# Performance work log

Hardware: AMD Instinct MI355X
Metric: run time of the kernel (lower is better)

## Reference

```python
import jax, jax.numpy as jnp
import numpy as np

NB_CODE = 1024
N, CODE_DIM, T = 32, 512, 2048


def setup_inputs() -> dict:
    key = jax.random.key(0)
    k1, k2 = jax.random.split(key)
    x = jax.random.normal(k1, (N, CODE_DIM, T), dtype=jnp.float32)
    codebook = jax.random.normal(k2, (NB_CODE, CODE_DIM), dtype=jnp.float32)
    return {"x": x, "codebook": codebook}


def reference(x, codebook):
    n, c, t = x.shape
    # preprocess: 'n c t -> (n t) c'
    xf = jnp.transpose(x, (0, 2, 1)).reshape(n * t, c)  # (NT, C)
    dist = (
        jnp.sum(xf * xf, axis=-1, keepdims=True)
        - 2.0 * jnp.matmul(xf, codebook.T)
        + jnp.sum(codebook * codebook, axis=-1)[None, :]
    )
    # gumbel_sample(-distance) with training=False -> plain argmax(-dist) = argmin(dist)
    code_idx = jnp.argmin(dist, axis=-1)  # (NT,) int32
    # dequantize: embedding gather
    x_d = codebook[code_idx]  # (NT, C)
    # compute_perplexity (eval path)
    counts = jax.ops.segment_sum(
        jnp.ones_like(code_idx, dtype=jnp.float32), code_idx, num_segments=NB_CODE
    )
    prob = counts / jnp.sum(counts)
    perplexity = jnp.exp(-jnp.sum(prob * jnp.log(prob + 1e-7)))
    # commit loss against detached quantized codes
    commit_loss = jnp.mean(jnp.square(xf - jax.lax.stop_gradient(x_d)))
    # straight-through estimator
    x_st = xf + jax.lax.stop_gradient(x_d - xf)
    x_out = jnp.transpose(x_st.reshape(n, t, c), (0, 2, 1))  # (N, C, T)
    return x_out, commit_loss, perplexity
```

## Files before the change

### kernel.cpp

```cpp
#include <hip/hip_runtime.h>
#include <stdint.h>

#define N_  32
#define C_  512
#define T_  2048
#define NB  1024
#define NT  (N_ * T_)
#define GB_S 129

typedef _Float16 h8 __attribute__((ext_vector_type(8)));
typedef _Float16 h4 __attribute__((ext_vector_type(4)));
typedef float    f4 __attribute__((ext_vector_type(4)));

#define WS_COMMIT   0
#define WS_SUMSQ    8
#define WS_COUNTS   64
#define WS_CNORM    4224
#define WS_RMIN     8320
#define WS_CBH      532608
#define WS_CBL      1581184
#define WS_XTH      2629760
#define WS_XTL      69738624
#define WS_NEED     136847488ull

__device__ __forceinline__ void gll16(const void* g, void* l) {
    __builtin_amdgcn_global_load_lds((const __attribute__((address_space(1))) void*)g,
                                     (__attribute__((address_space(3))) void*)l, 16, 0, 0);
}

__global__ void k_initA(unsigned* ws32, unsigned long long* rmin) {
    int g = blockIdx.x * 256 + threadIdx.x;
    if (g < 1040) ws32[g] = 0u;
    rmin[g] = 0xFFFFFFFFFFFFFFFFull;
}

__global__ void k_initS(unsigned* ws32) {
    int g = blockIdx.x * 256 + threadIdx.x;
    if (g < 1040) ws32[g] = 0u;
}

__global__ void k_codenorm(const float* __restrict__ cb, float* __restrict__ cnorm) {
    int j = blockIdx.x * 256 + threadIdx.x;
    const float* r = cb + (size_t)j * C_;
    float s = 0.f;
    for (int i = 0; i < C_; i += 4) {
        float4 v = *(const float4*)&r[i];
        s = fmaf(v.x, v.x, s); s = fmaf(v.y, v.y, s);
        s = fmaf(v.z, v.z, s); s = fmaf(v.w, v.w, s);
    }
    cnorm[j] = s;
}

__global__ void k_cvt_cb(const float* __restrict__ cb,
                         _Float16* __restrict__ cbh, _Float16* __restrict__ cbl) {
    int t = blockIdx.x * 256 + threadIdx.x;
    float4 v = *(const float4*)&cb[(size_t)t * 4];
    h4 hi, lo;
    hi.x = (_Float16)v.x; lo.x = (_Float16)(v.x - (float)hi.x);
    hi.y = (_Float16)v.y; lo.y = (_Float16)(v.y - (float)hi.y);
    hi.z = (_Float16)v.z; lo.z = (_Float16)(v.z - (float)hi.z);
    hi.w = (_Float16)v.w; lo.w = (_Float16)(v.w - (float)hi.w);
    *(h4*)&cbh[(size_t)t * 4] = hi;
    *(h4*)&cbl[(size_t)t * 4] = lo;
}

__global__ __launch_bounds__(256)
void k_xt(const float* __restrict__ x,
          _Float16* __restrict__ xth, _Float16* __restrict__ xtl,
          float* __restrict__ sumsq) {
    __shared__ float Ls[64 * 68];
    __shared__ float sred[4];
    const int bx = blockIdx.x;
    const int n = bx >> 8;
    const int cblk = (bx >> 5) & 7, tblk = bx & 31;
    const int c0 = cblk * 64, t0 = tblk * 64;
    const int tid = threadIdx.x;
    #pragma unroll
    for (int ld = 0; ld < 4; ++ld) {
        int idx = tid + ld * 256;
        int cc = idx >> 4, t4 = (idx & 15) << 2;
        float4 v = *(const float4*)&x[((size_t)n * C_ + c0 + cc) * T_ + t0 + t4];
        *(float4*)&Ls[cc * 68 + t4] = v;
    }
    __syncthreads();
    const int tt = tid >> 2, cs = (tid & 3) * 16;
    h8 hi0, hi1, lo0, lo1;
    float ss = 0.f;
    #pragma unroll
    for (int j = 0; j < 8; ++j) {
        float f = Ls[(cs + j) * 68 + tt];
        ss = fmaf(f, f, ss);
        _Float16 h = (_Float16)f;
        hi0[j] = h; lo0[j] = (_Float16)(f - (float)h);
    }
    #pragma unroll
    for (int j = 0; j < 8; ++j) {
        float f = Ls[(cs + 8 + j) * 68 + tt];
        ss = fmaf(f, f, ss);
        _Float16 h = (_Float16)f;
        hi1[j] = h; lo1[j] = (_Float16)(f - (float)h);
    }
    const size_t dst = ((size_t)n * T_ + t0 + tt) * C_ + c0 + cs;
    *(h8*)&xth[dst] = hi0; *(h8*)&xth[dst + 8] = hi1;
    *(h8*)&xtl[dst] = lo0; *(h8*)&xtl[dst + 8] = lo1;
    #pragma unroll
    for (int off = 32; off; off >>= 1) ss += __shfl_down(ss, off, 64);
    if ((tid & 63) == 0) sred[tid >> 6] = ss;
    __syncthreads();
    if (tid == 0) atomicAdd(sumsq, sred[0] + sred[1] + sred[2] + sred[3]);
}

__global__ __launch_bounds__(512, 2)
void k_gemm(const _Float16* __restrict__ xth, const _Float16* __restrict__ xtl,
            const _Float16* __restrict__ cbh, const _Float16* __restrict__ cbl,
            const float* __restrict__ cnorm, unsigned long long* __restrict__ rmin) {
    __shared__ __attribute__((aligned(128))) char smc[131072];
    const int tid = threadIdx.x;
    const int l = tid & 63, w = tid >> 6;
    const int q = l >> 4, r = l & 15;

    const int bid = blockIdx.x;
    const int swz = (bid & 7) * 128 + (bid >> 3);
    const int mb = swz >> 2, nb = swz & 3;

    const char* xthc = (const char*)xth;
    const char* xtlc = (const char*)xtl;
    const char* cbhc = (const char*)cbh;
    const char* cblc = (const char*)cbl;

    const int g16 = l >> 2;
    const int sslot = ((l & 3) ^ (g16 & 3)) << 4;
    const int s = w >> 1;
    const int rhalf = (w & 1) * 128;
    const char* sbase = (s == 0) ? xthc : (s == 1) ? xtlc : (s == 2) ? cbhc : cblc;
    const int rowblk = (s < 2) ? (mb * 256) : (nb * 256);
    const size_t srcOff = ((size_t)(rowblk + rhalf + g16)) * 1024 + sslot;
    const int ldsOff = s * 16384 + rhalf * 64;

    const int wmi = w & 3, wni = w >> 2;
    const int slq = (q ^ (r & 3)) << 4;
    const int aoffb = (wmi * 64 + r) * 64 + slq;
    const int boffb = 32768 + (wni * 128 + r) * 64 + slq;

    f4 acc[4][8];
    #pragma unroll
    for (int i = 0; i < 4; ++i)
        #pragma unroll
        for (int j = 0; j < 8; ++j) acc[i][j] = (f4){0.f, 0.f, 0.f, 0.f};

#define STAGE_T(tt, bb) { \
    const char* sp_ = sbase + srcOff + (tt) * 64; \
    char* dp_ = smc + (bb) + ldsOff; \
    _Pragma("unroll") \
    for (int c_ = 0; c_ < 8; ++c_) gll16(sp_ + c_ * 16384, dp_ + c_ * 1024); }

    STAGE_T(0, 0);
    asm volatile("s_waitcnt vmcnt(0)" ::: "memory");
    __builtin_amdgcn_s_barrier();

    int b0 = 0;
    #pragma unroll 2
    for (int t = 0; t < 16; ++t) {
        if (t < 15) STAGE_T(t + 1, b0 ^ 65536);
        h8 ah[4], al[4];
        #pragma unroll
        for (int mf = 0; mf < 4; ++mf) {
            ah[mf] = *(const h8*)(smc + b0 + aoffb + mf * 1024);
            al[mf] = *(const h8*)(smc + b0 + 16384 + aoffb + mf * 1024);
        }
        __builtin_amdgcn_s_setprio(1);
        #pragma unroll
        for (int nf = 0; nf < 8; ++nf) {
            h8 bhf = *(const h8*)(smc + b0 + boffb + nf * 1024);
            h8 blf = *(const h8*)(smc + b0 + 16384 + boffb + nf * 1024);
            #pragma unroll
            for (int mf = 0; mf < 4; ++mf) {
                acc[mf][nf] = __builtin_amdgcn_mfma_f32_16x16x32_f16(ah[mf], bhf, acc[mf][nf], 0, 0, 0);
                acc[mf][nf] = __builtin_amdgcn_mfma_f32_16x16x32_f16(al[mf], bhf, acc[mf][nf], 0, 0, 0);
                acc[mf][nf] = __builtin_amdgcn_mfma_f32_16x16x32_f16(ah[mf], blf, acc[mf][nf], 0, 0, 0);
            }
        }
        __builtin_amdgcn_s_setprio(0);
        if (t < 15) {
            asm volatile("s_waitcnt vmcnt(0)" ::: "memory");
            __builtin_amdgcn_s_barrier();
            b0 ^= 65536;
        }
    }
#undef STAGE_T

    const int codeBase = nb * 256 + wni * 128;
    const int rowBase  = mb * 256 + wmi * 64;
    float cn[8];
    #pragma unroll
    for (int nf = 0; nf < 8; ++nf) cn[nf] = cnorm[codeBase + nf * 16 + r];

    #pragma unroll
    for (int mf = 0; mf < 4; ++mf) {
        #pragma unroll
        for (int rg = 0; rg < 4; ++rg) {
            unsigned long long best = 0xFFFFFFFFFFFFFFFFull;
            #pragma unroll
            for (int nf = 0; nf < 8; ++nf) {
                float sc = fmaf(-2.0f, acc[mf][nf][rg], cn[nf]);
                unsigned u = __float_as_uint(sc);
                u = (u & 0x80000000u) ? ~u : (u | 0x80000000u);
                unsigned long long key =
                    ((unsigned long long)u << 32) | (unsigned)(codeBase + nf * 16 + r);
                best = key < best ? key : best;
            }
            #pragma unroll
            for (int off = 1; off < 16; off <<= 1) {
                unsigned long long o = __shfl_xor(best, off, 64);
                best = o < best ? o : best;
            }
            if (r == 0)
                atomicMin(&rmin[rowBase + mf * 16 + q * 4 + rg], best);
        }
    }
}

__global__ __launch_bounds__(256)
void k_post(const float* __restrict__ cb,
            const unsigned long long* __restrict__ rmin,
            float* __restrict__ out, float* __restrict__ commitAcc,
            int* __restrict__ counts) {
    __shared__ float gbuf[64 * GB_S];
    __shared__ int sidx[128];
    __shared__ float red[4];
    const int bid = blockIdx.x;
    const int tid = threadIdx.x;
    const size_t r0 = (size_t)bid * 128;
    const int n  = (int)(r0 >> 11);
    const int t0 = (int)(r0 & 2047);
    const size_t xbase = (size_t)n * C_ * T_ + t0;

    float sc = 0.f;
    if (tid < 128) {
        unsigned long long key = rmin[r0 + tid];
        int code = (int)(key & 0xFFFFFFFFull);
        sidx[tid] = code;
        atomicAdd(&counts[code], 1);
        unsigned up = (unsigned)(key >> 32);
        unsigned ub = (up & 0x80000000u) ? (up & 0x7FFFFFFFu) : ~up;
        sc = __uint_as_float(ub);
    }
    #pragma unroll
    for (int off = 32; off; off >>= 1) sc += __shfl_down(sc, off, 64);
    if ((tid & 63) == 0) red[tid >> 6] = sc;
    __syncthreads();
    if (tid == 0) atomicAdd(commitAcc, red[0] + red[1] + red[2] + red[3]);

    const int tl   = tid >> 1;
    const int half = tid & 1;
    const int tcol  = tid & 127;
    const int chalf = tid >> 7;

    for (int c0 = 0; c0 < C_; c0 += 64) {
        __syncthreads();
        const int code = sidx[tl];
        const float* src = &cb[(size_t)code * C_ + c0 + half * 32];
        #pragma unroll
        for (int qq = 0; qq < 8; ++qq) {
            float4 v = *(const float4*)&src[qq * 4];
            const int cc = half * 32 + qq * 4;
            gbuf[(cc + 0) * GB_S + tl] = v.x;
            gbuf[(cc + 1) * GB_S + tl] = v.y;
            gbuf[(cc + 2) * GB_S + tl] = v.z;
            gbuf[(cc + 3) * GB_S + tl] = v.w;
        }
        __syncthreads();
        #pragma unroll 8
        for (int i = 0; i < 32; ++i) {
            const int cc = i * 2 + chalf;
            const size_t gidx = xbase + (size_t)(c0 + cc) * T_ + tcol;
            out[gidx] = gbuf[cc * GB_S + tcol];
        }
    }
}

__global__ void k_final(const int* __restrict__ counts,
                        const float* __restrict__ commitAcc,
                        const float* __restrict__ sumsq,
                        float* __restrict__ out) {
    __shared__ float red[4];
    int tid = threadIdx.x;
    float s = 0.f;
    for (int j = tid; j < NB; j += 256) {
        float p = (float)counts[j] * (1.0f / (float)NT);
        s += p * logf(p + 1e-7f);
    }
    #pragma unroll
    for (int off = 32; off; off >>= 1) s += __shfl_down(s, off, 64);
    if ((tid & 63) == 0) red[tid >> 6] = s;
    __syncthreads();
    if (tid == 0) {
        float H = red[0] + red[1] + red[2] + red[3];
        out[(size_t)NT * C_]     = (commitAcc[0] + sumsq[0]) * (1.0f / ((float)NT * (float)C_));
        out[(size_t)NT * C_ + 1] = expf(-H);
    }
}

#define BM  128
#define BN  128
#define BK  16
#define AS_S 128
#define BS_S 132

__global__ __launch_bounds__(256, 4)
void k_main_fb(const float* __restrict__ x, const float* __restrict__ cb,
               const float* __restrict__ cnorm, float* __restrict__ out,
               float* __restrict__ commitAcc, int* __restrict__ counts) {
    __shared__ float smem[8256];
    __shared__ unsigned long long rmin[BM];
    __shared__ int sidx[BM];
    __shared__ float red[4];

    float* As = smem;
    float* Bs = smem + BK * AS_S;

    const int bid = blockIdx.x;
    const int n   = bid >> 4;
    const int t0  = (bid & 15) << 7;
    const int tid = threadIdx.x;
    const int tx  = tid & 15;
    const int ty  = tid >> 4;

    if (tid < BM) rmin[tid] = 0xFFFFFFFFFFFFFFFFull;

    const size_t xbase = (size_t)n * C_ * T_ + t0;

    for (int ch = 0; ch < NB / BN; ++ch) {
        const int j0 = ch * BN;
        float acc[2][2][4][4];
        #pragma unroll
        for (int a0 = 0; a0 < 2; ++a0)
            #pragma unroll
            for (int a1 = 0; a1 < 2; ++a1)
                #pragma unroll
                for (int a2 = 0; a2 < 4; ++a2)
                    #pragma unroll
                    for (int a3 = 0; a3 < 4; ++a3) acc[a0][a1][a2][a3] = 0.f;

        for (int kb = 0; kb < C_ / BK; ++kb) {
            const int k0 = kb * BK;
            __syncthreads();
            {
                const int kk = tid >> 5;
                const int m4 = (tid & 31) << 2;
                float4 a0v = *(const float4*)&x[xbase + (size_t)(k0 + kk) * T_ + m4];
                float4 a1v = *(const float4*)&x[xbase + (size_t)(k0 + kk + 8) * T_ + m4];
                *(float4*)&As[kk * AS_S + m4] = a0v;
                *(float4*)&As[(kk + 8) * AS_S + m4] = a1v;
                const int j  = tid >> 2;
                const int kq = (tid & 3) << 2;
                float4 b0v = *(const float4*)&cb[(size_t)(j0 + j) * C_ + k0 + kq];
                float4 b1v = *(const float4*)&cb[(size_t)(j0 + j + 64) * C_ + k0 + kq];
                Bs[(kq + 0) * BS_S + j] = b0v.x;
                Bs[(kq + 1) * BS_S + j] = b0v.y;
                Bs[(kq + 2) * BS_S + j] = b0v.z;
                Bs[(kq + 3) * BS_S + j] = b0v.w;
                Bs[(kq + 0) * BS_S + j + 64] = b1v.x;
                Bs[(kq + 1) * BS_S + j + 64] = b1v.y;
                Bs[(kq + 2) * BS_S + j + 64] = b1v.z;
                Bs[(kq + 3) * BS_S + j + 64] = b1v.w;
            }
            __syncthreads();
            #pragma unroll
            for (int kk = 0; kk < BK; ++kk) {
                float4 aL = *(const float4*)&As[kk * AS_S + (ty << 2)];
                float4 aH = *(const float4*)&As[kk * AS_S + 64 + (ty << 2)];
                float4 bL = *(const float4*)&Bs[kk * BS_S + (tx << 2)];
                float4 bH = *(const float4*)&Bs[kk * BS_S + 64 + (tx << 2)];
                float av[2][4] = {{aL.x, aL.y, aL.z, aL.w}, {aH.x, aH.y, aH.z, aH.w}};
                float bv[2][4] = {{bL.x, bL.y, bL.z, bL.w}, {bH.x, bH.y, bH.z, bH.w}};
                #pragma unroll
                for (int ih = 0; ih < 2; ++ih)
                    #pragma unroll
                    for (int i = 0; i < 4; ++i)
                        #pragma unroll
                        for (int jh = 0; jh < 2; ++jh)
                            #pragma unroll
                            for (int j = 0; j < 4; ++j)
                                acc[ih][jh][i][j] = fmaf(av[ih][i], bv[jh][j], acc[ih][jh][i][j]);
            }
        }

        float cnj[2][4];
        #pragma unroll
        for (int jh = 0; jh < 2; ++jh)
            #pragma unroll
            for (int j = 0; j < 4; ++j)
                cnj[jh][j] = cnorm[j0 + jh * 64 + (tx << 2) + j];

        #pragma unroll
        for (int ih = 0; ih < 2; ++ih) {
            #pragma unroll
            for (int i = 0; i < 4; ++i) {
                const int row = ih * 64 + (ty << 2) + i;
                unsigned long long best = 0xFFFFFFFFFFFFFFFFull;
                #pragma unroll
                for (int jh = 0; jh < 2; ++jh) {
                    #pragma unroll
                    for (int j = 0; j < 4; ++j) {
                        const int code = j0 + jh * 64 + (tx << 2) + j;
                        float s = fmaf(-2.0f, acc[ih][jh][i][j], cnj[jh][j]);
                        unsigned u = __float_as_uint(s);
                        u = (u & 0x80000000u) ? ~u : (u | 0x80000000u);
                        unsigned long long key =
                            ((unsigned long long)u << 32) | (unsigned)code;
                        best = key < best ? key : best;
                    }
                }
                #pragma unroll
                for (int off = 8; off; off >>= 1) {
                    unsigned long long o = __shfl_down(best, off, 16);
                    best = o < best ? o : best;
                }
                if (tx == 0) {
                    unsigned long long cur = rmin[row];
                    rmin[row] = best < cur ? best : cur;
                }
            }
        }
    }

    __syncthreads();
    if (tid < BM) {
        int code = (int)(rmin[tid] & 0xFFFFFFFFull);
        sidx[tid] = code;
        atomicAdd(&counts[code], 1);
    }
    __syncthreads();

    float* gbuf = smem;
    const int tl   = tid >> 1;
    const int half = tid & 1;
    const int tcol  = tid & 127;
    const int chalf = tid >> 7;
    float commit = 0.f;

    for (int c0 = 0; c0 < C_; c0 += 64) {
        __syncthreads();
        const int code = sidx[tl];
        const float* src = &cb[(size_t)code * C_ + c0 + half * 32];
        #pragma unroll
        for (int qq = 0; qq < 8; ++qq) {
            float4 v = *(const float4*)&src[qq * 4];
            const int cc = half * 32 + qq * 4;
            gbuf[(cc + 0) * GB_S + tl] = v.x;
            gbuf[(cc + 1) * GB_S + tl] = v.y;
            gbuf[(cc + 2) * GB_S + tl] = v.z;
            gbuf[(cc + 3) * GB_S + tl] = v.w;
        }
        __syncthreads();
        #pragma unroll 8
        for (int i = 0; i < 32; ++i) {
            const int cc = i * 2 + chalf;
            const size_t gidx = xbase + (size_t)(c0 + cc) * T_ + tcol;
            float g  = gbuf[cc * GB_S + tcol];
            float xv = x[gidx];
            out[gidx] = g;
            float d = xv - g;
            commit = fmaf(d, d, commit);
        }
    }

    #pragma unroll
    for (int off = 32; off; off >>= 1) commit += __shfl_down(commit, off, 64);
    if ((tid & 63) == 0) red[tid >> 6] = commit;
    __syncthreads();
    if (tid == 0) atomicAdd(commitAcc, red[0] + red[1] + red[2] + red[3]);
}

extern "C" void kernel_launch(void* const* d_in, const int* in_sizes, int n_in,
                              void* d_out, int out_size, void* d_ws, size_t ws_size,
                              hipStream_t stream) {
    const float* x  = (const float*)d_in[0];
    const float* cb = (const float*)d_in[1];
    float* out = (float*)d_out;

    char* ws = (char*)d_ws;
    float* commitAcc = (float*)(ws + WS_COMMIT);
    float* sumsq     = (float*)(ws + WS_SUMSQ);
    int*   counts    = (int*)(ws + WS_COUNTS);
    float* cnorm     = (float*)(ws + WS_CNORM);
    unsigned long long* rmin = (unsigned long long*)(ws + WS_RMIN);
    _Float16* cbh = (_Float16*)(ws + WS_CBH);
    _Float16* cbl = (_Float16*)(ws + WS_CBL);
    _Float16* xth = (_Float16*)(ws + WS_XTH);
    _Float16* xtl = (_Float16*)(ws + WS_XTL);

    if (ws_size >= WS_NEED) {
        k_initA<<<256, 256, 0, stream>>>((unsigned*)ws, rmin);
        k_codenorm<<<4, 256, 0, stream>>>(cb, cnorm);
        k_cvt_cb<<<512, 256, 0, stream>>>(cb, cbh, cbl);
        k_xt<<<8192, 256, 0, stream>>>(x, xth, xtl, sumsq);
        k_gemm<<<1024, 512, 0, stream>>>(xth, xtl, cbh, cbl, cnorm, rmin);
        k_post<<<512, 256, 0, stream>>>(cb, rmin, out, commitAcc, counts);
        k_final<<<1, 256, 0, stream>>>(counts, commitAcc, sumsq, out);
    } else {
        k_initS<<<5, 256, 0, stream>>>((unsigned*)ws);
        k_codenorm<<<4, 256, 0, stream>>>(cb, cnorm);
        k_main_fb<<<512, 256, 0, stream>>>(x, cb, cnorm, out, commitAcc, counts);
        k_final<<<1, 256, 0, stream>>>(counts, commitAcc, sumsq, out);
    }
}
```

Measured before the change: 540.1 us.

## Fuse argmin GEMM with gather/post stage and merge codebook preprocessing kernels

The GEMM kernel now gives each block a full 128-row strip and loops over all 1024 codes in 8 chunks, keeping a running argmin in registers. This removes the global atomicMin rmin buffer, its init, and the separate k_post launch, since the block does the gather, straight-through output and commit-loss accumulation itself. The codebook conversion, norm and workspace zeroing are merged into one launch. In exchange the grid drops from 1024 blocks of 512 threads to 512 blocks of 256 threads with smaller per-wave tiles, which may lower MFMA utilisation. The A tile is also reloaded from global memory for each code chunk.

```diff
diff --git a/kernel.cpp b/kernel.cpp
--- a/kernel.cpp
+++ b/kernel.cpp
@@ -28,10 +28,34 @@
                                      (__attribute__((address_space(3))) void*)l, 16, 0, 0);
 }
 
-__global__ void k_initA(unsigned* ws32, unsigned long long* rmin) {
-    int g = blockIdx.x * 256 + threadIdx.x;
-    if (g < 1040) ws32[g] = 0u;
-    rmin[g] = 0xFFFFFFFFFFFFFFFFull;
+__global__ __launch_bounds__(256)
+void k_pre(const float* __restrict__ cb, float* __restrict__ cnorm,
+           _Float16* __restrict__ cbh, _Float16* __restrict__ cbl,
+           unsigned* __restrict__ ws32) {
+    const int bid = blockIdx.x, tid = threadIdx.x;
+    if (bid < 512) {
+        int t = bid * 256 + tid;
+        float4 v = *(const float4*)&cb[(size_t)t * 4];
+        h4 hi, lo;
+        hi.x = (_Float16)v.x; lo.x = (_Float16)(v.x - (float)hi.x);
+        hi.y = (_Float16)v.y; lo.y = (_Float16)(v.y - (float)hi.y);
+        hi.z = (_Float16)v.z; lo.z = (_Float16)(v.z - (float)hi.z);
+        hi.w = (_Float16)v.w; lo.w = (_Float16)(v.w - (float)hi.w);
+        *(h4*)&cbh[(size_t)t * 4] = hi;
+        *(h4*)&cbl[(size_t)t * 4] = lo;
+    } else if (bid < 516) {
+        int j = (bid - 512) * 256 + tid;
+        const float* r = cb + (size_t)j * C_;
+        float s = 0.f;
+        for (int i = 0; i < C_; i += 4) {
+            float4 v = *(const float4*)&r[i];
+            s = fmaf(v.x, v.x, s); s = fmaf(v.y, v.y, s);
+            s = fmaf(v.z, v.z, s); s = fmaf(v.w, v.w, s);
+        }
+        cnorm[j] = s;
+    } else {
+        for (int g = tid; g < 1040; g += 256) ws32[g] = 0u;
+    }
 }
 
 __global__ void k_initS(unsigned* ws32) {
@@ -49,19 +73,6 @@
         s = fmaf(v.z, v.z, s); s = fmaf(v.w, v.w, s);
     }
     cnorm[j] = s;
-}
-
-__global__ void k_cvt_cb(const float* __restrict__ cb,
-                         _Float16* __restrict__ cbh, _Float16* __restrict__ cbl) {
-    int t = blockIdx.x * 256 + threadIdx.x;
-    float4 v = *(const float4*)&cb[(size_t)t * 4];
-    h4 hi, lo;
-    hi.x = (_Float16)v.x; lo.x = (_Float16)(v.x - (float)hi.x);
-    hi.y = (_Float16)v.y; lo.y = (_Float16)(v.y - (float)hi.y);
-    hi.z = (_Float16)v.z; lo.z = (_Float16)(v.z - (float)hi.z);
-    hi.w = (_Float16)v.w; lo.w = (_Float16)(v.w - (float)hi.w);
-    *(h4*)&cbh[(size_t)t * 4] = hi;
-    *(h4*)&cbl[(size_t)t * 4] = lo;
 }
 
 __global__ __launch_bounds__(256)
@@ -110,134 +121,133 @@
     if (tid == 0) atomicAdd(sumsq, sred[0] + sred[1] + sred[2] + sred[3]);
 }
 
-__global__ __launch_bounds__(512, 2)
+__global__ __launch_bounds__(256, 2)
 void k_gemm(const _Float16* __restrict__ xth, const _Float16* __restrict__ xtl,
             const _Float16* __restrict__ cbh, const _Float16* __restrict__ cbl,
-            const float* __restrict__ cnorm, unsigned long long* __restrict__ rmin) {
-    __shared__ __attribute__((aligned(128))) char smc[131072];
+            const float* __restrict__ cnorm, const float* __restrict__ cb,
+            float* __restrict__ out, float* __restrict__ commitAcc,
+            int* __restrict__ counts) {
+    __shared__ __attribute__((aligned(128))) char smc[65536];
+    __shared__ unsigned long long rminP[256];
+    __shared__ int sidx[128];
+    __shared__ float red[4];
+
     const int tid = threadIdx.x;
     const int l = tid & 63, w = tid >> 6;
     const int q = l >> 4, r = l & 15;
-
     const int bid = blockIdx.x;
-    const int swz = (bid & 7) * 128 + (bid >> 3);
-    const int mb = swz >> 2, nb = swz & 3;
-
-    const char* xthc = (const char*)xth;
-    const char* xtlc = (const char*)xtl;
-    const char* cbhc = (const char*)cbh;
-    const char* cblc = (const char*)cbl;
 
     const int g16 = l >> 2;
-    const int sslot = ((l & 3) ^ (g16 & 3)) << 4;
-    const int s = w >> 1;
-    const int rhalf = (w & 1) * 128;
-    const char* sbase = (s == 0) ? xthc : (s == 1) ? xtlc : (s == 2) ? cbhc : cblc;
-    const int rowblk = (s < 2) ? (mb * 256) : (nb * 256);
-    const size_t srcOff = ((size_t)(rowblk + rhalf + g16)) * 1024 + sslot;
-    const int ldsOff = s * 16384 + rhalf * 64;
-
-    const int wmi = w & 3, wni = w >> 2;
-    const int slq = (q ^ (r & 3)) << 4;
+    const int sslot = (((l & 3) ^ ((l >> 4) & 3)) << 4);
+    const char* sbase = (w == 0) ? (const char*)xth : (w == 1) ? (const char*)xtl
+                      : (w == 2) ? (const char*)cbh : (const char*)cbl;
+    const size_t aRow0 = (size_t)bid * 128;
+    const int ldsOff = w * 8192;
+
+    const int wmi = w >> 1, wni = w & 1;
+    const int slq = (q ^ ((r >> 2) & 3)) << 4;
     const int aoffb = (wmi * 64 + r) * 64 + slq;
-    const int boffb = 32768 + (wni * 128 + r) * 64 + slq;
-
-    f4 acc[4][8];
-    #pragma unroll
-    for (int i = 0; i < 4; ++i)
-        #pragma unroll
-        for (int j = 0; j < 8; ++j) acc[i][j] = (f4){0.f, 0.f, 0.f, 0.f};
-
-#define STAGE_T(tt, bb) { \
-    const char* sp_ = sbase + srcOff + (tt) * 64; \
+    const int boffb = 16384 + (wni * 64 + r) * 64 + slq;
+
+    unsigned long long best[4][4];
+    #pragma unroll
+    for (int mf = 0; mf < 4; ++mf)
+        #pragma unroll
+        for (int rg = 0; rg < 4; ++rg) best[mf][rg] = 0xFFFFFFFFFFFFFFFFull;
+
+#define STAGE_T(nb_, kb_, bb) { \
+    const size_t row0_ = (w < 2) ? (aRow0 + g16) : ((size_t)(nb_) * 128 + g16); \
+    const char* sp_ = sbase + row0_ * 1024 + (kb_) * 64 + sslot; \
     char* dp_ = smc + (bb) + ldsOff; \
     _Pragma("unroll") \
-    for (int c_ = 0; c_ < 8; ++c_) gll16(sp_ + c_ * 16384, dp_ + c_ * 1024); }
-
-    STAGE_T(0, 0);
-    asm volatile("s_waitcnt vmcnt(0)" ::: "memory");
-    __builtin_amdgcn_s_barrier();
+    for (int c_ = 0; c_ < 8; ++c_) gll16(sp_ + (size_t)c_ * 16384, dp_ + c_ * 1024); }
+
+    STAGE_T(0, 0, 0);
+    __syncthreads();
 
     int b0 = 0;
-    #pragma unroll 2
-    for (int t = 0; t < 16; ++t) {
-        if (t < 15) STAGE_T(t + 1, b0 ^ 65536);
-        h8 ah[4], al[4];
+    for (int nb = 0; nb < 8; ++nb) {
+        f4 acc[4][4];
+        #pragma unroll
+        for (int i = 0; i < 4; ++i)
+            #pragma unroll
+            for (int j = 0; j < 4; ++j) acc[i][j] = (f4){0.f, 0.f, 0.f, 0.f};
+
+        for (int kb = 0; kb < 16; ++kb) {
+            const int tn = nb * 16 + kb + 1;
+            if (tn < 128) { STAGE_T(tn >> 4, tn & 15, b0 ^ 32768); }
+
+            h8 ah[4], al[4];
+            #pragma unroll
+            for (int mf = 0; mf < 4; ++mf) {
+                ah[mf] = *(const h8*)(smc + b0 + aoffb + mf * 1024);
+                al[mf] = *(const h8*)(smc + b0 + 8192 + aoffb + mf * 1024);
+            }
+            __builtin_amdgcn_s_setprio(1);
+            #pragma unroll
+            for (int nf = 0; nf < 4; ++nf) {
+                h8 bhf = *(const h8*)(smc + b0 + boffb + nf * 1024);
+                h8 blf = *(const h8*)(smc + b0 + 8192 + boffb + nf * 1024);
+                #pragma unroll
+                for (int mf = 0; mf < 4; ++mf) {
+                    acc[mf][nf] = __builtin_amdgcn_mfma_f32_16x16x32_f16(ah[mf], bhf, acc[mf][nf], 0, 0, 0);
+                    acc[mf][nf] = __builtin_amdgcn_mfma_f32_16x16x32_f16(al[mf], bhf, acc[mf][nf], 0, 0, 0);
+                    acc[mf][nf] = __builtin_amdgcn_mfma_f32_16x16x32_f16(ah[mf], blf, acc[mf][nf], 0, 0, 0);
+                }
+            }
+            __builtin_amdgcn_s_setprio(0);
+
+            if (tn < 128) {
+                __syncthreads();
+                b0 ^= 32768;
+            }
+        }
+
+        const int codeBase = nb * 128 + wni * 64;
+        float cn[4];
+        #pragma unroll
+        for (int nf = 0; nf < 4; ++nf) cn[nf] = cnorm[codeBase + nf * 16 + r];
+
         #pragma unroll
         for (int mf = 0; mf < 4; ++mf) {
-            ah[mf] = *(const h8*)(smc + b0 + aoffb + mf * 1024);
-            al[mf] = *(const h8*)(smc + b0 + 16384 + aoffb + mf * 1024);
-        }
-        __builtin_amdgcn_s_setprio(1);
-        #pragma unroll
-        for (int nf = 0; nf < 8; ++nf) {
-            h8 bhf = *(const h8*)(smc + b0 + boffb + nf * 1024);
-            h8 blf = *(const h8*)(smc + b0 + 16384 + boffb + nf * 1024);
-            #pragma unroll
-            for (int mf = 0; mf < 4; ++mf) {
-                acc[mf][nf] = __builtin_amdgcn_mfma_f32_16x16x32_f16(ah[mf], bhf, acc[mf][nf], 0, 0, 0);
-                acc[mf][nf] = __builtin_amdgcn_mfma_f32_16x16x32_f16(al[mf], bhf, acc[mf][nf], 0, 0, 0);
-                acc[mf][nf] = __builtin_amdgcn_mfma_f32_16x16x32_f16(ah[mf], blf, acc[mf][nf], 0, 0, 0);
-            }
-        }
-        __builtin_amdgcn_s_setprio(0);
-        if (t < 15) {
-            asm volatile("s_waitcnt vmcnt(0)" ::: "memory");
-            __builtin_amdgcn_s_barrier();
-            b0 ^= 65536;
+            #pragma unroll
+            for (int rg = 0; rg < 4; ++rg) {
+                unsigned long long b = best[mf][rg];
+                #pragma unroll
+                for (int nf = 0; nf < 4; ++nf) {
+                    float sc = fmaf(-2.0f, acc[mf][nf][rg], cn[nf]);
+                    unsigned u = __float_as_uint(sc);
+                    u = (u & 0x80000000u) ? ~u : (u | 0x80000000u);
+                    unsigned long long key =
+                        ((unsigned long long)u << 32) | (unsigned)(codeBase + nf * 16 + r);
+                    b = key < b ? key : b;
+                }
+                best[mf][rg] = b;
+            }
         }
     }
 #undef STAGE_T
 
-    const int codeBase = nb * 256 + wni * 128;
-    const int rowBase  = mb * 256 + wmi * 64;
-    float cn[8];
-    #pragma unroll
-    for (int nf = 0; nf < 8; ++nf) cn[nf] = cnorm[codeBase + nf * 16 + r];
-
     #pragma unroll
     for (int mf = 0; mf < 4; ++mf) {
         #pragma unroll
         for (int rg = 0; rg < 4; ++rg) {
-            unsigned long long best = 0xFFFFFFFFFFFFFFFFull;
-            #pragma unroll
-            for (int nf = 0; nf < 8; ++nf) {
-                float sc = fmaf(-2.0f, acc[mf][nf][rg], cn[nf]);
-                unsigned u = __float_as_uint(sc);
-                u = (u & 0x80000000u) ? ~u : (u | 0x80000000u);
-                unsigned long long key =
-                    ((unsigned long long)u << 32) | (unsigned)(codeBase + nf * 16 + r);
-                best = key < best ? key : best;
-            }
+            unsigned long long b = best[mf][rg];
             #pragma unroll
             for (int off = 1; off < 16; off <<= 1) {
-                unsigned long long o = __shfl_xor(best, off, 64);
-                best = o < best ? o : best;
+                unsigned long long o = __shfl_xor(b, off, 64);
+                b = o < b ? o : b;
             }
             if (r == 0)
-                atomicMin(&rmin[rowBase + mf * 16 + q * 4 + rg], best);
-        }
-    }
-}
-
-__global__ __launch_bounds__(256)
-void k_post(const float* __restrict__ cb,
-            const unsigned long long* __restrict__ rmin,
-            float* __restrict__ out, float* __restrict__ commitAcc,
-            int* __restrict__ counts) {
-    __shared__ float gbuf[64 * GB_S];
-    __shared__ int sidx[128];
-    __shared__ float red[4];
-    const int bid = blockIdx.x;
-    const int tid = threadIdx.x;
-    const size_t r0 = (size_t)bid * 128;
-    const int n  = (int)(r0 >> 11);
-    const int t0 = (int)(r0 & 2047);
-    const size_t xbase = (size_t)n * C_ * T_ + t0;
+                rminP[wni * 128 + wmi * 64 + mf * 16 + q * 4 + rg] = b;
+        }
+    }
+    __syncthreads();
 
     float sc = 0.f;
     if (tid < 128) {
-        unsigned long long key = rmin[r0 + tid];
+        unsigned long long k0 = rminP[tid], k1 = rminP[128 + tid];
+        unsigned long long key = k1 < k0 ? k1 : k0;
         int code = (int)(key & 0xFFFFFFFFull);
         sidx[tid] = code;
         atomicAdd(&counts[code], 1);
@@ -250,6 +260,12 @@
     if ((tid & 63) == 0) red[tid >> 6] = sc;
     __syncthreads();
     if (tid == 0) atomicAdd(commitAcc, red[0] + red[1] + red[2] + red[3]);
+
+    const size_t r0 = (size_t)bid * 128;
+    const int n  = (int)(r0 >> 11);
+    const int t0 = (int)(r0 & 2047);
+    const size_t xbase = (size_t)n * C_ * T_ + t0;
+    float* gbuf = (float*)smc;
 
     const int tl   = tid >> 1;
     const int half = tid & 1;
@@ -485,19 +501,15 @@
     float* sumsq     = (float*)(ws + WS_SUMSQ);
     int*   counts    = (int*)(ws + WS_COUNTS);
     float* cnorm     = (float*)(ws + WS_CNORM);
-    unsigned long long* rmin = (unsigned long long*)(ws + WS_RMIN);
     _Float16* cbh = (_Float16*)(ws + WS_CBH);
     _Float16* cbl = (_Float16*)(ws + WS_CBL);
     _Float16* xth = (_Float16*)(ws + WS_XTH);
     _Float16* xtl = (_Float16*)(ws + WS_XTL);
 
     if (ws_size >= WS_NEED) {
-        k_initA<<<256, 256, 0, stream>>>((unsigned*)ws, rmin);
-        k_codenorm<<<4, 256, 0, stream>>>(cb, cnorm);
-        k_cvt_cb<<<512, 256, 0, stream>>>(cb, cbh, cbl);
+        k_pre<<<517, 256, 0, stream>>>(cb, cnorm, cbh, cbl, (unsigned*)ws);
         k_xt<<<8192, 256, 0, stream>>>(x, xth, xtl, sumsq);
-        k_gemm<<<1024, 512, 0, stream>>>(xth, xtl, cbh, cbl, cnorm, rmin);
-        k_post<<<512, 256, 0, stream>>>(cb, rmin, out, commitAcc, counts);
+        k_gemm<<<512, 256, 0, stream>>>(xth, xtl, cbh, cbl, cnorm, cb, out, commitAcc, counts);
         k_final<<<1, 256, 0, stream>>>(counts, commitAcc, sumsq, out);
     } else {
         k_initS<<<5, 256, 0, stream>>>((unsigned*)ws);
```

Measured after the change: 563.0 us. +4.2%, slower.

## Use 4-wave GEMM blocks with 128x128 per-wave tiles and fuse prep kernels

Applied to the files above, without the earlier changes.

The GEMM block drops from 8 waves to 4 waves. Each wave now computes a 128x128 output tile (8x8 MFMA fragments), which raises register reuse of the A and B fragments per LDS read. Staging is reorganised so each wave loads one full operand (hi or lo, x or codebook), and the main loop is manually unrolled into ping-pong buffers. Separately, the init, codebook norm and fp16 split kernels are merged into one launch to save launch overhead. The price is much higher register pressure (256 accumulator floats) and fewer waves to hide latency, with only one block per CU since LDS use is 128KB.

```diff
diff --git a/kernel.cpp b/kernel.cpp
--- a/kernel.cpp
+++ b/kernel.cpp
@@ -28,10 +28,37 @@
                                      (__attribute__((address_space(3))) void*)l, 16, 0, 0);
 }
 
-__global__ void k_initA(unsigned* ws32, unsigned long long* rmin) {
-    int g = blockIdx.x * 256 + threadIdx.x;
-    if (g < 1040) ws32[g] = 0u;
-    rmin[g] = 0xFFFFFFFFFFFFFFFFull;
+__global__ __launch_bounds__(256)
+void k_pre(const float* __restrict__ cb, float* __restrict__ cnorm,
+           _Float16* __restrict__ cbh, _Float16* __restrict__ cbl,
+           unsigned* __restrict__ ws32, unsigned long long* __restrict__ rmin) {
+    const int bid = blockIdx.x, tid = threadIdx.x;
+    if (bid < 512) {
+        int t = bid * 256 + tid;
+        float4 v = *(const float4*)&cb[(size_t)t * 4];
+        h4 hi, lo;
+        hi.x = (_Float16)v.x; lo.x = (_Float16)(v.x - (float)hi.x);
+        hi.y = (_Float16)v.y; lo.y = (_Float16)(v.y - (float)hi.y);
+        hi.z = (_Float16)v.z; lo.z = (_Float16)(v.z - (float)hi.z);
+        hi.w = (_Float16)v.w; lo.w = (_Float16)(v.w - (float)hi.w);
+        *(h4*)&cbh[(size_t)t * 4] = hi;
+        *(h4*)&cbl[(size_t)t * 4] = lo;
+    } else if (bid < 516) {
+        int j = (bid - 512) * 256 + tid;
+        const float* r = cb + (size_t)j * C_;
+        float s = 0.f;
+        for (int i = 0; i < C_; i += 4) {
+            float4 v = *(const float4*)&r[i];
+            s = fmaf(v.x, v.x, s); s = fmaf(v.y, v.y, s);
+            s = fmaf(v.z, v.z, s); s = fmaf(v.w, v.w, s);
+        }
+        cnorm[j] = s;
+    } else if (bid == 516) {
+        for (int g = tid; g < 1040; g += 256) ws32[g] = 0u;
+    } else {
+        int g = (bid - 517) * 256 + tid;
+        rmin[g] = 0xFFFFFFFFFFFFFFFFull;
+    }
 }
 
 __global__ void k_initS(unsigned* ws32) {
@@ -49,19 +76,6 @@
         s = fmaf(v.z, v.z, s); s = fmaf(v.w, v.w, s);
     }
     cnorm[j] = s;
-}
-
-__global__ void k_cvt_cb(const float* __restrict__ cb,
-                         _Float16* __restrict__ cbh, _Float16* __restrict__ cbl) {
-    int t = blockIdx.x * 256 + threadIdx.x;
-    float4 v = *(const float4*)&cb[(size_t)t * 4];
-    h4 hi, lo;
-    hi.x = (_Float16)v.x; lo.x = (_Float16)(v.x - (float)hi.x);
-    hi.y = (_Float16)v.y; lo.y = (_Float16)(v.y - (float)hi.y);
-    hi.z = (_Float16)v.z; lo.z = (_Float16)(v.z - (float)hi.z);
-    hi.w = (_Float16)v.w; lo.w = (_Float16)(v.w - (float)hi.w);
-    *(h4*)&cbh[(size_t)t * 4] = hi;
-    *(h4*)&cbl[(size_t)t * 4] = lo;
 }
 
 __global__ __launch_bounds__(256)
@@ -110,7 +124,7 @@
     if (tid == 0) atomicAdd(sumsq, sred[0] + sred[1] + sred[2] + sred[3]);
 }
 
-__global__ __launch_bounds__(512, 2)
+__global__ __launch_bounds__(256, 1)
 void k_gemm(const _Float16* __restrict__ xth, const _Float16* __restrict__ xtl,
             const _Float16* __restrict__ cbh, const _Float16* __restrict__ cbl,
             const float* __restrict__ cnorm, unsigned long long* __restrict__ rmin) {
@@ -123,80 +137,78 @@
     const int swz = (bid & 7) * 128 + (bid >> 3);
     const int mb = swz >> 2, nb = swz & 3;
 
-    const char* xthc = (const char*)xth;
-    const char* xtlc = (const char*)xtl;
-    const char* cbhc = (const char*)cbh;
-    const char* cblc = (const char*)cbl;
-
     const int g16 = l >> 2;
-    const int sslot = ((l & 3) ^ (g16 & 3)) << 4;
-    const int s = w >> 1;
-    const int rhalf = (w & 1) * 128;
-    const char* sbase = (s == 0) ? xthc : (s == 1) ? xtlc : (s == 2) ? cbhc : cblc;
-    const int rowblk = (s < 2) ? (mb * 256) : (nb * 256);
-    const size_t srcOff = ((size_t)(rowblk + rhalf + g16)) * 1024 + sslot;
-    const int ldsOff = s * 16384 + rhalf * 64;
-
-    const int wmi = w & 3, wni = w >> 2;
-    const int slq = (q ^ (r & 3)) << 4;
-    const int aoffb = (wmi * 64 + r) * 64 + slq;
+    const int sslot = (((l & 3) ^ ((l >> 3) & 3)) << 4);
+    const char* sbase = (w == 0) ? (const char*)xth : (w == 1) ? (const char*)xtl
+                      : (w == 2) ? (const char*)cbh : (const char*)cbl;
+    const size_t row0 = (w < 2) ? ((size_t)mb * 256) : ((size_t)nb * 256);
+    const size_t srcOff = (row0 + g16) * 1024 + sslot;
+    const int ldsOff = w * 16384;
+
+    const int wmi = w & 1, wni = w >> 1;
+    const int slq = (q ^ ((r >> 1) & 3)) << 4;
+    const int aoffb = (wmi * 128 + r) * 64 + slq;
     const int boffb = 32768 + (wni * 128 + r) * 64 + slq;
 
-    f4 acc[4][8];
-    #pragma unroll
-    for (int i = 0; i < 4; ++i)
+    f4 acc[8][8];
+    #pragma unroll
+    for (int i = 0; i < 8; ++i)
         #pragma unroll
         for (int j = 0; j < 8; ++j) acc[i][j] = (f4){0.f, 0.f, 0.f, 0.f};
 
-#define STAGE_T(tt, bb) { \
-    const char* sp_ = sbase + srcOff + (tt) * 64; \
+#define STAGE_T(kb_, bb) { \
+    const char* sp_ = sbase + srcOff + (size_t)(kb_) * 64; \
     char* dp_ = smc + (bb) + ldsOff; \
     _Pragma("unroll") \
-    for (int c_ = 0; c_ < 8; ++c_) gll16(sp_ + c_ * 16384, dp_ + c_ * 1024); }
+    for (int c_ = 0; c_ < 16; ++c_) gll16(sp_ + (size_t)c_ * 16384, dp_ + c_ * 1024); }
+
+#define COMPUTE(bb) { \
+    h8 ah[8], al[8]; \
+    _Pragma("unroll") \
+    for (int mf = 0; mf < 8; ++mf) { \
+        ah[mf] = *(const h8*)(smc + (bb) + aoffb + mf * 1024); \
+        al[mf] = *(const h8*)(smc + (bb) + 16384 + aoffb + mf * 1024); \
+    } \
+    __builtin_amdgcn_s_setprio(1); \
+    _Pragma("unroll") \
+    for (int nf = 0; nf < 8; ++nf) { \
+        h8 bhf = *(const h8*)(smc + (bb) + boffb + nf * 1024); \
+        h8 blf = *(const h8*)(smc + (bb) + 16384 + boffb + nf * 1024); \
+        _Pragma("unroll") \
+        for (int mf = 0; mf < 8; ++mf) { \
+            acc[mf][nf] = __builtin_amdgcn_mfma_f32_16x16x32_f16(ah[mf], bhf, acc[mf][nf], 0, 0, 0); \
+            acc[mf][nf] = __builtin_amdgcn_mfma_f32_16x16x32_f16(al[mf], bhf, acc[mf][nf], 0, 0, 0); \
+            acc[mf][nf] = __builtin_amdgcn_mfma_f32_16x16x32_f16(ah[mf], blf, acc[mf][nf], 0, 0, 0); \
+        } \
+    } \
+    __builtin_amdgcn_s_setprio(0); }
 
     STAGE_T(0, 0);
-    asm volatile("s_waitcnt vmcnt(0)" ::: "memory");
-    __builtin_amdgcn_s_barrier();
-
-    int b0 = 0;
-    #pragma unroll 2
-    for (int t = 0; t < 16; ++t) {
-        if (t < 15) STAGE_T(t + 1, b0 ^ 65536);
-        h8 ah[4], al[4];
-        #pragma unroll
-        for (int mf = 0; mf < 4; ++mf) {
-            ah[mf] = *(const h8*)(smc + b0 + aoffb + mf * 1024);
-            al[mf] = *(const h8*)(smc + b0 + 16384 + aoffb + mf * 1024);
-        }
-        __builtin_amdgcn_s_setprio(1);
-        #pragma unroll
-        for (int nf = 0; nf < 8; ++nf) {
-            h8 bhf = *(const h8*)(smc + b0 + boffb + nf * 1024);
-            h8 blf = *(const h8*)(smc + b0 + 16384 + boffb + nf * 1024);
-            #pragma unroll
-            for (int mf = 0; mf < 4; ++mf) {
-                acc[mf][nf] = __builtin_amdgcn_mfma_f32_16x16x32_f16(ah[mf], bhf, acc[mf][nf], 0, 0, 0);
-                acc[mf][nf] = __builtin_amdgcn_mfma_f32_16x16x32_f16(al[mf], bhf, acc[mf][nf], 0, 0, 0);
-                acc[mf][nf] = __builtin_amdgcn_mfma_f32_16x16x32_f16(ah[mf], blf, acc[mf][nf], 0, 0, 0);
-            }
-        }
-        __builtin_amdgcn_s_setprio(0);
-        if (t < 15) {
-            asm volatile("s_waitcnt vmcnt(0)" ::: "memory");
-            __builtin_amdgcn_s_barrier();
-            b0 ^= 65536;
+    __syncthreads();
+
+    for (int tp = 0; tp < 8; ++tp) {
+        STAGE_T(2 * tp + 1, 65536);
+        COMPUTE(0);
+        __syncthreads();
+        if (tp < 7) {
+            STAGE_T(2 * tp + 2, 0);
+            COMPUTE(65536);
+            __syncthreads();
+        } else {
+            COMPUTE(65536);
         }
     }
 #undef STAGE_T
+#undef COMPUTE
 
     const int codeBase = nb * 256 + wni * 128;
-    const int rowBase  = mb * 256 + wmi * 64;
+    const int rowBase  = mb * 256 + wmi * 128;
     float cn[8];
     #pragma unroll
     for (int nf = 0; nf < 8; ++nf) cn[nf] = cnorm[codeBase + nf * 16 + r];
 
     #pragma unroll
-    for (int mf = 0; mf < 4; ++mf) {
+    for (int mf = 0; mf < 8; ++mf) {
         #pragma unroll
         for (int rg = 0; rg < 4; ++rg) {
             unsigned long long best = 0xFFFFFFFFFFFFFFFFull;
@@ -492,11 +504,9 @@
     _Float16* xtl = (_Float16*)(ws + WS_XTL);
 
     if (ws_size >= WS_NEED) {
-        k_initA<<<256, 256, 0, stream>>>((unsigned*)ws, rmin);
-        k_codenorm<<<4, 256, 0, stream>>>(cb, cnorm);
-        k_cvt_cb<<<512, 256, 0, stream>>>(cb, cbh, cbl);
+        k_pre<<<773, 256, 0, stream>>>(cb, cnorm, cbh, cbl, (unsigned*)ws, rmin);
         k_xt<<<8192, 256, 0, stream>>>(x, xth, xtl, sumsq);
-        k_gemm<<<1024, 512, 0, stream>>>(xth, xtl, cbh, cbl, cnorm, rmin);
+        k_gemm<<<1024, 256, 0, stream>>>(xth, xtl, cbh, cbl, cnorm, rmin);
         k_post<<<512, 256, 0, stream>>>(cb, rmin, out, commitAcc, counts);
         k_final<<<1, 256, 0, stream>>>(counts, commitAcc, sumsq, out);
     } else {
```

New measurement: 793.8 us. +47.0%, slower.

## Fuse codebook preprocessing kernels and change LDS swizzle in GEMM

Applied to the files above, without the earlier changes.

Merges the workspace init, codebook-norm and codebook fp16 hi/lo split kernels into one launch with blocks partitioned by role. This removes two kernel launches and the gaps between them. Separately, the XOR swizzle used for LDS staging and fragment reads in the GEMM now keys on different row bits (row>>1 instead of row), aiming to cut LDS bank conflicts for the 64-byte row layout. The write and read swizzles must stay consistent, and they appear to be changed in matching ways.

```diff
diff --git a/kernel.cpp b/kernel.cpp
--- a/kernel.cpp
+++ b/kernel.cpp
@@ -28,10 +28,37 @@
                                      (__attribute__((address_space(3))) void*)l, 16, 0, 0);
 }
 
-__global__ void k_initA(unsigned* ws32, unsigned long long* rmin) {
-    int g = blockIdx.x * 256 + threadIdx.x;
-    if (g < 1040) ws32[g] = 0u;
-    rmin[g] = 0xFFFFFFFFFFFFFFFFull;
+__global__ __launch_bounds__(256)
+void k_pre(const float* __restrict__ cb, float* __restrict__ cnorm,
+           _Float16* __restrict__ cbh, _Float16* __restrict__ cbl,
+           unsigned* __restrict__ ws32, unsigned long long* __restrict__ rmin) {
+    const int bid = blockIdx.x, tid = threadIdx.x;
+    if (bid < 512) {
+        int t = bid * 256 + tid;
+        float4 v = *(const float4*)&cb[(size_t)t * 4];
+        h4 hi, lo;
+        hi.x = (_Float16)v.x; lo.x = (_Float16)(v.x - (float)hi.x);
+        hi.y = (_Float16)v.y; lo.y = (_Float16)(v.y - (float)hi.y);
+        hi.z = (_Float16)v.z; lo.z = (_Float16)(v.z - (float)hi.z);
+        hi.w = (_Float16)v.w; lo.w = (_Float16)(v.w - (float)hi.w);
+        *(h4*)&cbh[(size_t)t * 4] = hi;
+        *(h4*)&cbl[(size_t)t * 4] = lo;
+    } else if (bid < 516) {
+        int j = (bid - 512) * 256 + tid;
+        const float* r = cb + (size_t)j * C_;
+        float s = 0.f;
+        for (int i = 0; i < C_; i += 4) {
+            float4 v = *(const float4*)&r[i];
+            s = fmaf(v.x, v.x, s); s = fmaf(v.y, v.y, s);
+            s = fmaf(v.z, v.z, s); s = fmaf(v.w, v.w, s);
+        }
+        cnorm[j] = s;
+    } else if (bid == 516) {
+        for (int g = tid; g < 1040; g += 256) ws32[g] = 0u;
+    } else {
+        int g = (bid - 517) * 256 + tid;
+        rmin[g] = 0xFFFFFFFFFFFFFFFFull;
+    }
 }
 
 __global__ void k_initS(unsigned* ws32) {
@@ -49,19 +76,6 @@
         s = fmaf(v.z, v.z, s); s = fmaf(v.w, v.w, s);
     }
     cnorm[j] = s;
-}
-
-__global__ void k_cvt_cb(const float* __restrict__ cb,
-                         _Float16* __restrict__ cbh, _Float16* __restrict__ cbl) {
-    int t = blockIdx.x * 256 + threadIdx.x;
-    float4 v = *(const float4*)&cb[(size_t)t * 4];
-    h4 hi, lo;
-    hi.x = (_Float16)v.x; lo.x = (_Float16)(v.x - (float)hi.x);
-    hi.y = (_Float16)v.y; lo.y = (_Float16)(v.y - (float)hi.y);
-    hi.z = (_Float16)v.z; lo.z = (_Float16)(v.z - (float)hi.z);
-    hi.w = (_Float16)v.w; lo.w = (_Float16)(v.w - (float)hi.w);
-    *(h4*)&cbh[(size_t)t * 4] = hi;
-    *(h4*)&cbl[(size_t)t * 4] = lo;
 }
 
 __global__ __launch_bounds__(256)
@@ -129,7 +143,7 @@
     const char* cblc = (const char*)cbl;
 
     const int g16 = l >> 2;
-    const int sslot = ((l & 3) ^ (g16 & 3)) << 4;
+    const int sslot = ((l & 3) ^ ((l >> 3) & 3)) << 4;
     const int s = w >> 1;
     const int rhalf = (w & 1) * 128;
     const char* sbase = (s == 0) ? xthc : (s == 1) ? xtlc : (s == 2) ? cbhc : cblc;
@@ -138,7 +152,7 @@
     const int ldsOff = s * 16384 + rhalf * 64;
 
     const int wmi = w & 3, wni = w >> 2;
-    const int slq = (q ^ (r & 3)) << 4;
+    const int slq = (q ^ ((r >> 1) & 3)) << 4;
     const int aoffb = (wmi * 64 + r) * 64 + slq;
     const int boffb = 32768 + (wni * 128 + r) * 64 + slq;
 
@@ -492,9 +506,7 @@
     _Float16* xtl = (_Float16*)(ws + WS_XTL);
 
     if (ws_size >= WS_NEED) {
-        k_initA<<<256, 256, 0, stream>>>((unsigned*)ws, rmin);
-        k_codenorm<<<4, 256, 0, stream>>>(cb, cnorm);
-        k_cvt_cb<<<512, 256, 0, stream>>>(cb, cbh, cbl);
+        k_pre<<<773, 256, 0, stream>>>(cb, cnorm, cbh, cbl, (unsigned*)ws, rmin);
         k_xt<<<8192, 256, 0, stream>>>(x, xth, xtl, sumsq);
         k_gemm<<<1024, 512, 0, stream>>>(xth, xtl, cbh, cbl, cnorm, rmin);
         k_post<<<512, 256, 0, stream>>>(cb, rmin, out, commitAcc, counts);
```

Result: no change. 534.9 us (-1.0%).
